# Kernel tuning notes

Hardware: AMD Instinct MI355X
Metric: run time of the kernel (lower is better)

Reference implementation:

```python
import jax, jax.numpy as jnp
import numpy as np

HIDDEN = 1024
HEADS = 16
D_K = HIDDEN // HEADS
NEG_INF = -jnp.inf


def setup_inputs() -> dict:
    key = jax.random.key(0)
    ks = jax.random.split(key, 9)
    N, S = 4, 2048
    scale = 1.0 / np.sqrt(HIDDEN)
    x = jax.random.normal(ks[0], (N, S, HIDDEN), dtype=jnp.float32)
    attn_mask = jnp.ones((N, S), dtype=jnp.int32)
    Wq = jax.random.normal(ks[1], (HIDDEN, HIDDEN), dtype=jnp.float32) * scale
    bq = jnp.zeros((HIDDEN,), dtype=jnp.float32)
    Wk = jax.random.normal(ks[2], (HIDDEN, HIDDEN), dtype=jnp.float32) * scale
    bk = jnp.zeros((HIDDEN,), dtype=jnp.float32)
    Wv = jax.random.normal(ks[3], (HIDDEN, HIDDEN), dtype=jnp.float32) * scale
    bv = jnp.zeros((HIDDEN,), dtype=jnp.float32)
    Wp = jax.random.normal(ks[4], (HIDDEN, HIDDEN), dtype=jnp.float32) * scale
    bp = jnp.zeros((HIDDEN,), dtype=jnp.float32)
    return {"x": x, "attn_mask": attn_mask, "Wq": Wq, "bq": bq,
            "Wk": Wk, "bk": bk, "Wv": Wv, "bv": bv, "Wp": Wp, "bp": bp}


def reference(x, attn_mask, Wq, bq, Wk, bk, Wv, bv, Wp, bp):
    N, S, _ = x.shape
    H, dk = HEADS, D_K
    # torch nn.Linear: y = x @ W.T + b
    q = (x @ Wq.T + bq).reshape(N, S, H, dk).transpose(0, 2, 1, 3)  # (N,H,S,dk)
    k = (x @ Wk.T + bk).reshape(N, S, H, dk).transpose(0, 2, 1, 3)
    v = (x @ Wv.T + bv).reshape(N, S, H, dk).transpose(0, 2, 1, 3)
    attn = jnp.einsum('nhqd,nhkd->nhqk', q, k) / jnp.sqrt(jnp.float32(dk))
    mask = attn_mask.reshape(N, 1, 1, S)
    attn = jnp.where(mask == 0, NEG_INF, attn)
    attn = jax.nn.softmax(attn, axis=-1)
    # dropout is identity in eval mode
    y = jnp.einsum('nhqk,nhkd->nhqd', attn, v)  # (N,H,S,dk)
    y = y.transpose(0, 2, 1, 3).reshape(N, S, H * dk)
    return y @ Wp.T + bp
```

## Files before the change

kernel.cpp:

```cpp
#include <hip/hip_runtime.h>

typedef unsigned short u16;
typedef unsigned int u32;
typedef unsigned long long u64;
typedef __attribute__((ext_vector_type(8))) short bf16x8;
typedef __attribute__((ext_vector_type(4))) short bf16x4;
typedef __attribute__((ext_vector_type(4))) float f32x4;
typedef __attribute__((ext_vector_type(2))) unsigned int u32x2;

#define AS1(p) ((const __attribute__((address_space(1))) void*)(p))
#define AS3(p) ((__attribute__((address_space(3))) void*)(p))

__device__ __forceinline__ u16 f2bf(float f) {
    u32 u = __float_as_uint(f);
    u += 0x7fff + ((u >> 16) & 1);
    return (u16)(u >> 16);
}
__device__ __forceinline__ u32 pack2bf(float lo, float hi) {
    u32 a = __float_as_uint(lo) + 0x8000u;
    u32 b = __float_as_uint(hi) + 0x8000u;
    return __builtin_amdgcn_perm(b, a, 0x07060302);
}

__device__ __forceinline__ void async16(const u16* g, u16* l) {
    __builtin_amdgcn_global_load_lds(AS1(g), AS3(l), 16, 0, 0);
}

__global__ __launch_bounds__(256) void cvt_kernel(const float* __restrict__ src,
                                                  u16* __restrict__ dst, int n) {
    int idx = (blockIdx.x * 256 + threadIdx.x) * 8;
    if (idx >= n) return;
    float4 a = *(const float4*)(src + idx);
    float4 b = *(const float4*)(src + idx + 4);
    uint4 o;
    o.x = (u32)f2bf(a.x) | ((u32)f2bf(a.y) << 16);
    o.y = (u32)f2bf(a.z) | ((u32)f2bf(a.w) << 16);
    o.z = (u32)f2bf(b.x) | ((u32)f2bf(b.y) << 16);
    o.w = (u32)f2bf(b.z) | ((u32)f2bf(b.w) << 16);
    *(uint4*)(dst + idx) = o;
}

__global__ __launch_bounds__(256) void cvt4_kernel(
    const float* __restrict__ s0, const float* __restrict__ s1,
    const float* __restrict__ s2, const float* __restrict__ s3,
    u16* __restrict__ d0, u16* __restrict__ d1,
    u16* __restrict__ d2, u16* __restrict__ d3) {
    const float* s; u16* d;
    switch (blockIdx.y) {
        case 0:  s = s0; d = d0; break;
        case 1:  s = s1; d = d1; break;
        case 2:  s = s2; d = d2; break;
        default: s = s3; d = d3; break;
    }
    int idx = (blockIdx.x * 256 + threadIdx.x) * 8;
    float4 a = *(const float4*)(s + idx);
    float4 b = *(const float4*)(s + idx + 4);
    uint4 o;
    o.x = (u32)f2bf(a.x) | ((u32)f2bf(a.y) << 16);
    o.y = (u32)f2bf(a.z) | ((u32)f2bf(a.w) << 16);
    o.z = (u32)f2bf(b.x) | ((u32)f2bf(b.y) << 16);
    o.w = (u32)f2bf(b.z) | ((u32)f2bf(b.w) << 16);
    *(uint4*)(d + idx) = o;
}

__global__ __launch_bounds__(256, 2) void gemm_bt(
    const u16* __restrict__ A,
    const u16* __restrict__ Wa, const u16* __restrict__ Wb, const u16* __restrict__ Wc,
    const float* __restrict__ ba, const float* __restrict__ bb, const float* __restrict__ bc,
    void* oa, void* ob_, void* oc, int mode)
{
    constexpr int K = 1024;
    __shared__ u16 smem[128 * 132];
    u16* At = smem;
    u16* Wt = smem + 4096;

    const int tid = threadIdx.x;
    const int lane = tid & 63, wv = tid >> 6;
    const int l15 = lane & 15, quad = lane >> 4;
    const int wr = wv >> 1, wc = wv & 1;

    const int L = blockIdx.x + (blockIdx.y << 3) + (blockIdx.z << 9);
    const int g = L & 7;
    const int j = L >> 3;
    const int z = j >> 6;
    const int r = j & 63;
    const int m0 = ((g << 3) + (r & 7)) * 128;
    const int n0 = (r >> 3) * 128;

    const u16* W = (z == 0) ? Wa : ((z == 1) ? Wb : Wc);
    const float* bs = (z == 0) ? ba : ((z == 1) ? bb : bc);
    void* out = (z == 0) ? oa : ((z == 1) ? ob_ : oc);
    const bool swap_ = (mode == 1) || (z < 2);

    f32x4 acc[4][4];
#pragma unroll
    for (int i = 0; i < 4; ++i)
#pragma unroll
        for (int j2 = 0; j2 < 4; ++j2) acc[i][j2] = (f32x4)0.f;

    const int call0 = wv * 2;
    for (int kk = 0; kk < K; kk += 32) {
#pragma unroll
        for (int jj = 0; jj < 2; ++jj) {
            int c = (call0 + jj) * 64 + lane;
            int row = c >> 2;
            int ko = ((c & 3) ^ (row & 3)) * 8;
            async16(A + (size_t)(m0 + row) * K + kk + ko, &At[(call0 + jj) * 512 + lane * 8]);
            async16(W + (size_t)(n0 + row) * K + kk + ko, &Wt[(call0 + jj) * 512 + lane * 8]);
        }
        __syncthreads();

        bf16x8 af[4], wf[4];
#pragma unroll
        for (int t = 0; t < 4; ++t) {
            int rowa = wr * 64 + t * 16 + l15;
            af[t] = *(const bf16x8*)&At[rowa * 32 + ((quad ^ (rowa & 3)) * 8)];
            int rowb = wc * 64 + t * 16 + l15;
            wf[t] = *(const bf16x8*)&Wt[rowb * 32 + ((quad ^ (rowb & 3)) * 8)];
        }
        if (swap_) {
#pragma unroll
            for (int rt = 0; rt < 4; ++rt)
#pragma unroll
                for (int ct = 0; ct < 4; ++ct)
                    acc[rt][ct] = __builtin_amdgcn_mfma_f32_16x16x32_bf16(wf[ct], af[rt], acc[rt][ct], 0, 0, 0);
        } else {
#pragma unroll
            for (int rt = 0; rt < 4; ++rt)
#pragma unroll
                for (int ct = 0; ct < 4; ++ct)
                    acc[rt][ct] = __builtin_amdgcn_mfma_f32_16x16x32_bf16(af[rt], wf[ct], acc[rt][ct], 0, 0, 0);
        }
        __syncthreads();
    }

    if (mode == 1) {
#pragma unroll
        for (int rt = 0; rt < 4; ++rt)
#pragma unroll
            for (int ct = 0; ct < 4; ++ct) {
                int m_ = m0 + wr * 64 + rt * 16 + l15;
                int ob = n0 + wc * 64 + ct * 16 + quad * 4;
                float4 b4 = *(const float4*)&bs[ob];
                float4 v;
                v.x = acc[rt][ct][0] + b4.x;
                v.y = acc[rt][ct][1] + b4.y;
                v.z = acc[rt][ct][2] + b4.z;
                v.w = acc[rt][ct][3] + b4.w;
                *(float4*)((float*)out + (size_t)m_ * 1024 + ob) = v;
            }
        return;
    }

    const int n = m0 >> 11, s0 = m0 & 2047;
    if (z < 2) {
        const float qs = (z == 0) ? 0.18033688011112042f : 1.0f;
#pragma unroll
        for (int rt = 0; rt < 4; ++rt)
#pragma unroll
            for (int ct = 0; ct < 4; ++ct) {
                int ml = wr * 64 + rt * 16 + l15;
                int ol = wc * 64 + ct * 16 + quad * 4;
                float4 b4 = *(const float4*)&bs[n0 + ol];
                float v0 = (acc[rt][ct][0] + b4.x) * qs;
                float v1 = (acc[rt][ct][1] + b4.y) * qs;
                float v2 = (acc[rt][ct][2] + b4.z) * qs;
                float v3 = (acc[rt][ct][3] + b4.w) * qs;
                u32x2 pv = { pack2bf(v0, v1), pack2bf(v2, v3) };
                *(u32x2*)&smem[ml * 132 + ol] = pv;
            }
        __syncthreads();
        const int h0 = n0 >> 6;
#pragma unroll
        for (int p = 0; p < 8; ++p) {
            int hh = p >> 2, qq = p & 3;
            int m = qq * 32 + (tid >> 3), d = (tid & 7) * 8;
            bf16x8 vv = *(const bf16x8*)&smem[m * 132 + hh * 64 + d];
            u16* dst = (u16*)out + ((size_t)((n * 16 + h0 + hh) * 2048 + s0 + m)) * 64 + d;
            *(bf16x8*)dst = vv;
        }
    } else {
#pragma unroll
        for (int rt = 0; rt < 4; ++rt)
#pragma unroll
            for (int ct = 0; ct < 4; ++ct) {
                int ol = wc * 64 + ct * 16 + l15;
                int ml = wr * 64 + rt * 16 + quad * 4;
                float b = bs[n0 + ol];
                float v0 = acc[rt][ct][0] + b;
                float v1 = acc[rt][ct][1] + b;
                float v2 = acc[rt][ct][2] + b;
                float v3 = acc[rt][ct][3] + b;
                u32x2 pv = { pack2bf(v0, v1), pack2bf(v2, v3) };
                *(u32x2*)&smem[ol * 132 + ml] = pv;
            }
        __syncthreads();
#pragma unroll
        for (int p = 0; p < 8; ++p) {
            int o = p * 16 + (tid >> 4), ms = (tid & 15) * 8;
            bf16x8 vv = *(const bf16x8*)&smem[o * 132 + ms];
            int og = n0 + o;
            int h = og >> 6, d = og & 63;
            u16* dst = (u16*)out + ((size_t)((n * 16 + h) * 64 + d)) * 2048 + s0 + ms;
            *(bf16x8*)dst = vv;
        }
    }
}

__global__ __launch_bounds__(256) void attn_kernel(
    const u16* __restrict__ Q, const u16* __restrict__ K_,
    const u16* __restrict__ VT, const int* __restrict__ mask,
    u16* __restrict__ Y)
{
    constexpr int S = 2048, DK = 64, STR = 72;
    __shared__ u16 Kt[64 * STR];
    __shared__ u16 Vt[64 * STR];
    __shared__ u16 Pq[8][16 * STR];
    __shared__ int mtile[64];

    const int tid = threadIdx.x;
    const int lane = tid & 63, w = tid >> 6;
    const int l15 = lane & 15, quad = lane >> 4;
    const int nh = blockIdx.y;
    const int n = nh >> 4, h = nh & 15;
    const int qbase = blockIdx.x * 128;

    const u16* Qh = Q + (size_t)nh * S * DK;
    const u16* Kh = K_ + (size_t)nh * S * DK;
    const u16* Vh = VT + (size_t)nh * DK * S;

    bf16x8 qf[2][2];
#pragma unroll
    for (int nt = 0; nt < 2; ++nt)
#pragma unroll
        for (int st = 0; st < 2; ++st)
            qf[nt][st] = *(const bf16x8*)(Qh + (size_t)(qbase + w * 32 + nt * 16 + l15) * DK + st * 32 + quad * 8);

    f32x4 o[4][2];
#pragma unroll
    for (int dt = 0; dt < 4; ++dt)
#pragma unroll
        for (int nt = 0; nt < 2; ++nt) o[dt][nt] = (f32x4)0.f;
    float lsum[2] = {0.f, 0.f};

    const int r0 = tid >> 3, c8 = (tid & 7) * 8;
    bf16x8 rk0 = *(const bf16x8*)(Kh + (size_t)r0 * 64 + c8);
    bf16x8 rk1 = *(const bf16x8*)(Kh + (size_t)(r0 + 32) * 64 + c8);
    bf16x8 rv0 = *(const bf16x8*)(Vh + (size_t)r0 * S + c8);
    bf16x8 rv1 = *(const bf16x8*)(Vh + (size_t)(r0 + 32) * S + c8);
    int mreg = 0;
    if (tid < 64) mreg = mask[n * S + tid];

    for (int it = 0; it < 32; ++it) {
        *(bf16x8*)&Kt[r0 * STR + c8] = rk0;
        *(bf16x8*)&Kt[(r0 + 32) * STR + c8] = rk1;
        *(bf16x8*)&Vt[r0 * STR + c8] = rv0;
        *(bf16x8*)&Vt[(r0 + 32) * STR + c8] = rv1;
        if (tid < 64) mtile[tid] = mreg;
        __syncthreads();

        const int kkn = ((it + 1) << 6) & (S - 1);
        rk0 = *(const bf16x8*)(Kh + (size_t)(kkn + r0) * 64 + c8);
        rk1 = *(const bf16x8*)(Kh + (size_t)(kkn + r0 + 32) * 64 + c8);
        rv0 = *(const bf16x8*)(Vh + (size_t)r0 * S + kkn + c8);
        rv1 = *(const bf16x8*)(Vh + (size_t)(r0 + 32) * S + kkn + c8);
        if (tid < 64) mreg = mask[n * S + kkn + tid];

        f32x4 sacc[4][2];
#pragma unroll
        for (int jt = 0; jt < 4; ++jt)
#pragma unroll
            for (int nt = 0; nt < 2; ++nt) sacc[jt][nt] = (f32x4)0.f;
#pragma unroll
        for (int st = 0; st < 2; ++st)
#pragma unroll
            for (int jt = 0; jt < 4; ++jt) {
                bf16x8 kf = *(const bf16x8*)&Kt[(jt * 16 + l15) * STR + st * 32 + quad * 8];
                sacc[jt][0] = __builtin_amdgcn_mfma_f32_16x16x32_bf16(kf, qf[0][st], sacc[jt][0], 0, 0, 0);
                sacc[jt][1] = __builtin_amdgcn_mfma_f32_16x16x32_bf16(kf, qf[1][st], sacc[jt][1], 0, 0, 0);
            }

        const bool fast = (__ballot(mtile[lane] != 0) == ~0ull);
        if (!fast) {
#pragma unroll
            for (int jt = 0; jt < 4; ++jt)
#pragma unroll
                for (int r = 0; r < 4; ++r) {
                    int mv = mtile[jt * 16 + quad * 4 + r];
#pragma unroll
                    for (int nt = 0; nt < 2; ++nt)
                        if (mv == 0) sacc[jt][nt][r] = -1e30f;
                }
        }

#pragma unroll
        for (int nt = 0; nt < 2; ++nt) {
            float ps = 0.f;
#pragma unroll
            for (int jt = 0; jt < 4; ++jt) {
                float e0 = __builtin_amdgcn_exp2f(sacc[jt][nt][0]);
                float e1 = __builtin_amdgcn_exp2f(sacc[jt][nt][1]);
                float e2 = __builtin_amdgcn_exp2f(sacc[jt][nt][2]);
                float e3 = __builtin_amdgcn_exp2f(sacc[jt][nt][3]);
                ps += (e0 + e1) + (e2 + e3);
                u32x2 pv = { pack2bf(e0, e1), pack2bf(e2, e3) };
                *(u32x2*)&Pq[w * 2 + nt][l15 * STR + jt * 16 + quad * 4] = pv;
            }
            lsum[nt] += ps;
        }

#pragma unroll
        for (int kt = 0; kt < 2; ++kt) {
            bf16x8 p0 = *(const bf16x8*)&Pq[w * 2 + 0][l15 * STR + kt * 32 + quad * 8];
            bf16x8 p1 = *(const bf16x8*)&Pq[w * 2 + 1][l15 * STR + kt * 32 + quad * 8];
#pragma unroll
            for (int dt = 0; dt < 4; ++dt) {
                bf16x8 vf = *(const bf16x8*)&Vt[(dt * 16 + l15) * STR + kt * 32 + quad * 8];
                o[dt][0] = __builtin_amdgcn_mfma_f32_16x16x32_bf16(vf, p0, o[dt][0], 0, 0, 0);
                o[dt][1] = __builtin_amdgcn_mfma_f32_16x16x32_bf16(vf, p1, o[dt][1], 0, 0, 0);
            }
        }
        __syncthreads();
    }

#pragma unroll
    for (int nt = 0; nt < 2; ++nt) {
        float ls = lsum[nt];
        ls += __shfl_xor(ls, 16);
        ls += __shfl_xor(ls, 32);
        float rl = (ls > 0.f) ? 1.f / ls : 0.f;
        int qi = qbase + w * 32 + nt * 16 + l15;
#pragma unroll
        for (int dt = 0; dt < 4; ++dt) {
            u32x2 pv = { pack2bf(o[dt][nt][0] * rl, o[dt][nt][1] * rl),
                         pack2bf(o[dt][nt][2] * rl, o[dt][nt][3] * rl) };
            size_t base = ((size_t)(n * 2048 + qi)) * 1024 + h * 64 + dt * 16 + quad * 4;
            *(u32x2*)(Y + base) = pv;
        }
    }
}

extern "C" void kernel_launch(void* const* d_in, const int* in_sizes, int n_in,
                              void* d_out, int out_size, void* d_ws, size_t ws_size,
                              hipStream_t stream) {
    const float* x  = (const float*)d_in[0];
    const int* mask = (const int*)d_in[1];
    const float* Wq = (const float*)d_in[2];
    const float* bq = (const float*)d_in[3];
    const float* Wk = (const float*)d_in[4];
    const float* bk = (const float*)d_in[5];
    const float* Wv = (const float*)d_in[6];
    const float* bv = (const float*)d_in[7];
    const float* Wp = (const float*)d_in[8];
    const float* bp = (const float*)d_in[9];

    char* ws = (char*)d_ws;
    u16* xb  = (u16*)(ws);
    u16* wqb = (u16*)(ws + (16u << 20));
    u16* wkb = (u16*)(ws + (18u << 20));
    u16* wvb = (u16*)(ws + (20u << 20));
    u16* wpb = (u16*)(ws + (22u << 20));
    u16* Qb  = (u16*)(ws + (24u << 20));
    u16* Kb  = (u16*)(ws + (40u << 20));
    u16* Vb  = (u16*)(ws + (56u << 20));
    u16* Yb  = (u16*)(ws + (72u << 20));

    cvt_kernel<<<4096, 256, 0, stream>>>(x, xb, 8388608);
    cvt4_kernel<<<dim3(512, 4), 256, 0, stream>>>(Wq, Wk, Wv, Wp, wqb, wkb, wvb, wpb);

    gemm_bt<<<dim3(8, 64, 3), 256, 0, stream>>>(xb, wqb, wkb, wvb, bq, bk, bv,
                                                (void*)Qb, (void*)Kb, (void*)Vb, 0);

    attn_kernel<<<dim3(16, 64), 256, 0, stream>>>(Qb, Kb, Vb, mask, Yb);

    gemm_bt<<<dim3(8, 64, 1), 256, 0, stream>>>(Yb, wpb, wpb, wpb, bp, bp, bp,
                                                d_out, d_out, d_out, 1);
}
```

Baseline: 314.3 us.

## Keep P in registers via permlane swaps, remap blocks, and set MFMA priority

The attention kernel no longer round-trips the softmax probabilities through shared memory. It packs them with v_cvt_pk_bf16_f32 and rearranges them into the MFMA operand layout with permlane32/16 swaps, which removes LDS writes and reads and frees the Pq shared buffer, raising possible occupancy. It also remaps block indices so that consecutive blocks spread across heads or XCDs, and raises wave priority around the MFMA sections. The risks are that the lane permutation mapping must exactly match the old LDS layout, and that the bf16 rounding mode changes from the custom rounding to the hardware conversion.

Measured after the change: 304.2 us. 1.03x faster.

```diff
diff --git a/kernel.cpp b/kernel.cpp
--- a/kernel.cpp
+++ b/kernel.cpp
@@ -20,6 +20,11 @@
     u32 a = __float_as_uint(lo) + 0x8000u;
     u32 b = __float_as_uint(hi) + 0x8000u;
     return __builtin_amdgcn_perm(b, a, 0x07060302);
+}
+__device__ __forceinline__ u32 cvtpk(float lo, float hi) {
+    u32 r;
+    asm("v_cvt_pk_bf16_f32 %0, %1, %2" : "=v"(r) : "v"(lo), "v"(hi));
+    return r;
 }
 
 __device__ __forceinline__ void async16(const u16* g, u16* l) {
@@ -215,15 +220,17 @@
     constexpr int S = 2048, DK = 64, STR = 72;
     __shared__ u16 Kt[64 * STR];
     __shared__ u16 Vt[64 * STR];
-    __shared__ u16 Pq[8][16 * STR];
     __shared__ int mtile[64];
 
     const int tid = threadIdx.x;
     const int lane = tid & 63, w = tid >> 6;
     const int l15 = lane & 15, quad = lane >> 4;
-    const int nh = blockIdx.y;
+
+    const int L = blockIdx.x + (blockIdx.y << 4);
+    const int vb = (L & 7) * 128 + (L >> 3);
+    const int nh = vb >> 4;
     const int n = nh >> 4, h = nh & 15;
-    const int qbase = blockIdx.x * 128;
+    const int qbase = (vb & 15) * 128;
 
     const u16* Qh = Q + (size_t)nh * S * DK;
     const u16* Kh = K_ + (size_t)nh * S * DK;
@@ -271,6 +278,7 @@
         for (int jt = 0; jt < 4; ++jt)
 #pragma unroll
             for (int nt = 0; nt < 2; ++nt) sacc[jt][nt] = (f32x4)0.f;
+        __builtin_amdgcn_s_setprio(1);
 #pragma unroll
         for (int st = 0; st < 2; ++st)
 #pragma unroll
@@ -279,6 +287,7 @@
                 sacc[jt][0] = __builtin_amdgcn_mfma_f32_16x16x32_bf16(kf, qf[0][st], sacc[jt][0], 0, 0, 0);
                 sacc[jt][1] = __builtin_amdgcn_mfma_f32_16x16x32_bf16(kf, qf[1][st], sacc[jt][1], 0, 0, 0);
             }
+        __builtin_amdgcn_s_setprio(0);
 
         const bool fast = (__ballot(mtile[lane] != 0) == ~0ull);
         if (!fast) {
@@ -293,9 +302,11 @@
                 }
         }
 
+        bf16x8 pb[2][2];
 #pragma unroll
         for (int nt = 0; nt < 2; ++nt) {
             float ps = 0.f;
+            u32 pkx[4], pky[4];
 #pragma unroll
             for (int jt = 0; jt < 4; ++jt) {
                 float e0 = __builtin_amdgcn_exp2f(sacc[jt][nt][0]);
@@ -303,23 +314,36 @@
                 float e2 = __builtin_amdgcn_exp2f(sacc[jt][nt][2]);
                 float e3 = __builtin_amdgcn_exp2f(sacc[jt][nt][3]);
                 ps += (e0 + e1) + (e2 + e3);
-                u32x2 pv = { pack2bf(e0, e1), pack2bf(e2, e3) };
-                *(u32x2*)&Pq[w * 2 + nt][l15 * STR + jt * 16 + quad * 4] = pv;
+                pkx[jt] = cvtpk(e0, e1);
+                pky[jt] = cvtpk(e2, e3);
             }
             lsum[nt] += ps;
-        }
-
+#pragma unroll
+            for (int kt = 0; kt < 2; ++kt) {
+                auto rX = __builtin_amdgcn_permlane32_swap(pkx[2 * kt], pkx[2 * kt + 1], false, false);
+                auto rY = __builtin_amdgcn_permlane32_swap(pky[2 * kt], pky[2 * kt + 1], false, false);
+                auto sX = __builtin_amdgcn_permlane16_swap(rX[0], rX[1], false, false);
+                auto sY = __builtin_amdgcn_permlane16_swap(rY[0], rY[1], false, false);
+                union { u32 u[4]; bf16x8 v; } pu;
+                pu.u[0] = sX[0];
+                pu.u[1] = sY[0];
+                pu.u[2] = sX[1];
+                pu.u[3] = sY[1];
+                pb[nt][kt] = pu.v;
+            }
+        }
+
+        __builtin_amdgcn_s_setprio(1);
 #pragma unroll
         for (int kt = 0; kt < 2; ++kt) {
-            bf16x8 p0 = *(const bf16x8*)&Pq[w * 2 + 0][l15 * STR + kt * 32 + quad * 8];
-            bf16x8 p1 = *(const bf16x8*)&Pq[w * 2 + 1][l15 * STR + kt * 32 + quad * 8];
 #pragma unroll
             for (int dt = 0; dt < 4; ++dt) {
                 bf16x8 vf = *(const bf16x8*)&Vt[(dt * 16 + l15) * STR + kt * 32 + quad * 8];
-                o[dt][0] = __builtin_amdgcn_mfma_f32_16x16x32_bf16(vf, p0, o[dt][0], 0, 0, 0);
-                o[dt][1] = __builtin_amdgcn_mfma_f32_16x16x32_bf16(vf, p1, o[dt][1], 0, 0, 0);
-            }
-        }
+                o[dt][0] = __builtin_amdgcn_mfma_f32_16x16x32_bf16(vf, pb[0][kt], o[dt][0], 0, 0, 0);
+                o[dt][1] = __builtin_amdgcn_mfma_f32_16x16x32_bf16(vf, pb[1][kt], o[dt][1], 0, 0, 0);
+            }
+        }
+        __builtin_amdgcn_s_setprio(0);
         __syncthreads();
     }
 
```
